# Performance work log

Hardware: AMD Instinct MI355X
Metric: run time of the kernel (lower is better)

Reference implementation:

```python
import jax, jax.numpy as jnp
import numpy as np

N = 8192          # number of bodies
BOX = 112.0       # world size chosen so expected #colliding pairs ~ 4N
EPS = 1e-12


def setup_inputs() -> dict:
    key = jax.random.key(0)
    k1, k2 = jax.random.split(key)
    centers = jax.random.uniform(k1, (N, 2), dtype=jnp.float32) * BOX
    radii = 0.5 + 0.5 * jax.random.uniform(k2, (N,), dtype=jnp.float32)
    return {"centers": centers, "radii": radii, "limit_broad": 4 * N, "limit_narrow": N}


def reference(centers, radii, limit_broad, limit_narrow):
    n = centers.shape[0]
    # ---- broad phase: all-pairs AABB overlap (AABB = center +/- radius) ----
    dc = jnp.abs(centers[:, None, :] - centers[None, :, :])      # [N,N,2]
    rsum = radii[:, None] + radii[None, :]                        # [N,N]
    overlap = jnp.all(dc <= rsum[..., None], axis=-1)             # [N,N]
    idx = jnp.arange(n)
    mask = overlap & (idx[:, None] < idx[None, :])                # i < j, as in _check_aabb_collision
    # compaction to a fixed limit of 4N candidate pairs (-1 = empty slot)
    flat = jnp.nonzero(mask.reshape(-1), size=limit_broad, fill_value=-1)[0]
    valid_b = flat >= 0
    safe = jnp.where(valid_b, flat, 0)
    pi, pj = safe // n, safe % n                                  # [4N]
    # ---- narrow phase: exact circle penetration on the candidates ----
    d = centers[pj] - centers[pi]                                 # [4N,2]
    dist = jnp.sqrt(jnp.sum(d * d, axis=-1) + EPS)                # [4N]
    depth = radii[pi] + radii[pj] - dist                          # [4N]
    pen = d / dist[:, None] * depth[:, None]                      # penetration vector [4N,2]
    hit = valid_b & (depth > 0)
    # second compaction: keep at most N actually-penetrating pairs
    sel = jnp.nonzero(hit, size=limit_narrow, fill_value=-1)[0]
    vsel = sel >= 0
    ssafe = jnp.where(vsel, sel, 0)
    si, sj = pi[ssafe], pj[ssafe]                                 # [N]
    delta = 0.5 * pen[ssafe] * vsel[:, None].astype(centers.dtype)
    # ---- resolve: scatter: push bodies apart by half the penetration each ----
    new_centers = centers.at[si].add(-delta).at[sj].add(delta)
    return new_centers
```

## Files before the change

### kernel.cpp

```cpp
#include <hip/hip_runtime.h>


constexpr int NB = 8192;
constexpr int GRID_DIM = 56;
constexpr int NCELLS = GRID_DIM * GRID_DIM;
constexpr int CAP = 20;
constexpr int BPB = 28;
constexpr int TPB9 = BPB * 9;
constexpr int NBLK9 = (NB + BPB - 1) / BPB;
constexpr float INV_CELL = 0.5f;
constexpr float EPS = 1e-12f;
constexpr int INF = 0x7fffffff;

constexpr int O_CCOUNT = 0;
constexpr int O_CSUM   = O_CCOUNT + NCELLS;
constexpr int O_BSUM   = O_CSUM + 32;
constexpr int O_SPEC   = O_BSUM + 32;
constexpr int O_POL    = O_SPEC + 8;
constexpr int O_COMB   = O_POL + NB / 4;
constexpr int O_CELLS  = (O_COMB + NB + 3) & ~3;
constexpr int MEMSET_INTS = O_SPEC + 8;

__device__ __forceinline__ int cell_of(float v) {
    int c = (int)(v * INV_CELL);
    return c > GRID_DIM - 1 ? GRID_DIM - 1 : (c < 0 ? 0 : c);
}

__device__ __forceinline__ int wave_incl_scan(int v, int lane) {
#pragma unroll
    for (int off = 1; off < 64; off <<= 1) {
        int y = __shfl_up(v, off);
        if (lane >= off) v += y;
    }
    return v;
}

__global__ void fill_kernel(const float2* __restrict__ centers,
                            const float* __restrict__ radii,
                            int* __restrict__ ccount,
                            float4* __restrict__ cells) {
    const int t = blockIdx.x * blockDim.x + threadIdx.x;
    if (t >= NB) return;
    const float2 c = centers[t];
    const int cell = cell_of(c.y) * GRID_DIM + cell_of(c.x);
    const int slot = atomicAdd(&ccount[cell], 1);
    if (slot < CAP)
        cells[cell * CAP + slot] = make_float4(c.x, c.y, radii[t], __int_as_float(t));
}

__global__ __launch_bounds__(256) void count_kernel(
        const float2* __restrict__ centers, const float* __restrict__ radii,
        const int* __restrict__ ccount, const float4* __restrict__ cells,
        int* __restrict__ comb, int* __restrict__ csum, int* __restrict__ bsum) {
    __shared__ int sh_c[256];
    __shared__ int sh_s[BPB];
    const int tid = threadIdx.x;
    const int local = tid / 9, cellk = tid - local * 9;
    const int b = blockIdx.x * BPB + local;
    int rc = 0, hc = 0;
    if (tid < TPB9 && b < NB) {
        const float2 ci = centers[b];
        const float ri = radii[b];
        const int cx = cell_of(ci.x), cy = cell_of(ci.y);
        const int xx = cx - 1 + cellk % 3, yy = cy - 1 + cellk / 3;
        if (xx >= 0 && xx < GRID_DIM && yy >= 0 && yy < GRID_DIM) {
            const int c = yy * GRID_DIM + xx;
            const int n = min(ccount[c], CAP);
            const float4* p = cells + c * CAP;
            for (int k = 0; k < n; ++k) {
                const float4 o = p[k];
                if (__float_as_int(o.w) <= b) continue;
                const float rs = ri + o.z;
                const float dx = o.x - ci.x, dy = o.y - ci.y;
                if (fabsf(dx) <= rs && fabsf(dy) <= rs) {
                    ++rc;
                    if (rs - sqrtf(dx * dx + dy * dy + EPS) > 0.f) ++hc;
                }
            }
        }
    }
    sh_c[tid] = (rc << 8) | hc;
    __syncthreads();
    if (cellk == 0 && tid < TPB9) {
        int s = 0;
#pragma unroll
        for (int k = 0; k < 9; ++k) s += sh_c[tid + k];
        if (b < NB) comb[b] = s;
        sh_s[local] = (b < NB) ? s : 0;
    }
    __syncthreads();
    if (tid == 0) {
        const int chunk0 = (blockIdx.x * BPB) >> 8;
        int sA = 0, sB = 0;
#pragma unroll
        for (int l = 0; l < BPB; ++l) {
            const int v = sh_s[l];
            const int w = (v >> 8 << 16) | (v & 0xff);
            if (((blockIdx.x * BPB + l) >> 8) == chunk0) sA += w; else sB += w;
        }
        atomicAdd(&bsum[chunk0], sA >> 16);
        atomicAdd(&csum[chunk0], sA & 0xffff);
        if (sB) {
            atomicAdd(&bsum[chunk0 + 1], sB >> 16);
            atomicAdd(&csum[chunk0 + 1], sB & 0xffff);
        }
    }
}

__device__ int2 pair_rank(const int* ccount, const float4* cells,
                          float xi, float yi, float ri, int i, int j, int blim) {
    const int cx = cell_of(xi), cy = cell_of(yi);
    const int x0 = max(cx - 1, 0), x1 = min(cx + 1, GRID_DIM - 1);
    const int y0 = max(cy - 1, 0), y1 = min(cy + 1, GRID_DIM - 1);
    int brank = 0, hrank = 0;
    for (int yy = y0; yy <= y1; ++yy)
        for (int xx = x0; xx <= x1; ++xx) {
            const int c = yy * GRID_DIM + xx;
            const int n = min(ccount[c], CAP);
            for (int k = 0; k < n; ++k) {
                const float4 o2 = cells[c * CAP + k];
                const int j2 = __float_as_int(o2.w);
                if (j2 <= i || j2 >= j) continue;
                const float rs2 = ri + o2.z;
                const float dx2 = o2.x - xi, dy2 = o2.y - yi;
                if (!(fabsf(dx2) <= rs2 && fabsf(dy2) <= rs2)) continue;
                ++brank;
                if (rs2 - sqrtf(dx2 * dx2 + dy2 * dy2 + EPS) > 0.f) {
                    if (blim == INF) ++hrank;
                    else {
                        int b2 = 0;
                        for (int yb = y0; yb <= y1; ++yb)
                            for (int xb = x0; xb <= x1; ++xb) {
                                const int cb2 = yb * GRID_DIM + xb;
                                const int nb2 = min(ccount[cb2], CAP);
                                for (int k2 = 0; k2 < nb2; ++k2) {
                                    const float4 o3 = cells[cb2 * CAP + k2];
                                    const int j3 = __float_as_int(o3.w);
                                    if (j3 <= i || j3 >= j2) continue;
                                    const float rs3 = ri + o3.z;
                                    if (fabsf(o3.x - xi) <= rs3 && fabsf(o3.y - yi) <= rs3)
                                        ++b2;
                                }
                            }
                        if (b2 < blim) ++hrank;
                    }
                }
            }
        }
    return make_int2(brank, hrank);
}

__device__ int slow_boundary_hits(const int* ccount, const float4* cells,
                                  const float2* centers, const float* radii,
                                  int i, int lim) {
    const float2 ci = centers[i];
    const float ri = radii[i];
    const int cx = cell_of(ci.x), cy = cell_of(ci.y);
    const int x0 = max(cx - 1, 0), x1 = min(cx + 1, GRID_DIM - 1);
    const int y0 = max(cy - 1, 0), y1 = min(cy + 1, GRID_DIM - 1);
    int h = 0;
    for (int yy = y0; yy <= y1; ++yy)
        for (int xx = x0; xx <= x1; ++xx) {
            const int c = yy * GRID_DIM + xx;
            const int n = min(ccount[c], CAP);
            for (int k = 0; k < n; ++k) {
                const float4 o = cells[c * CAP + k];
                const int j = __float_as_int(o.w);
                if (j <= i) continue;
                const float rs = ri + o.z, dx = o.x - ci.x, dy = o.y - ci.y;
                if (!(fabsf(dx) <= rs && fabsf(dy) <= rs)) continue;
                if (rs - sqrtf(dx * dx + dy * dy + EPS) <= 0.f) continue;
                const int2 r = pair_rank(ccount, cells, ci.x, ci.y, ri, i, j, INF);
                if (r.x < lim) ++h;
            }
        }
    return h;
}

__global__ __launch_bounds__(256) void pol_kernel(
        const float2* __restrict__ centers, const float* __restrict__ radii,
        const int* __restrict__ ccount, const float4* __restrict__ cells,
        const int* __restrict__ comb,
        const int* __restrict__ csum, const int* __restrict__ bsum,
        const int* __restrict__ LBp, const int* __restrict__ LNp,
        unsigned char* __restrict__ pol, int* __restrict__ spec) {
    __shared__ int sh_cs[32], sh_bs[32], wsum[4];
    const int tid = threadIdx.x, lane = tid & 63, wid = tid >> 6;
    const int blk = blockIdx.x;
    const int r = blk * 256 + tid;
    if (tid < 32) { sh_cs[tid] = csum[tid]; sh_bs[tid] = bsum[tid]; }
    __syncthreads();
    int hbase = 0, bbase = 0, btotal = 0;
#pragma unroll
    for (int c = 0; c < 32; ++c) {
        btotal += sh_bs[c];
        if (c < blk) { hbase += sh_cs[c]; bbase += sh_bs[c]; }
    }
    const int LB = *LBp, LN = *LNp;
    const int v = comb[r];
    const int rc = v >> 8, hr = v & 0xff;
    const int pk = (rc << 16) | hr;
    int incl = wave_incl_scan(pk, lane);
    if (lane == 63) wsum[wid] = incl;
    __syncthreads();
    if (wid == 0) {
        const int orig = (lane < 4) ? wsum[lane] : 0;
        const int inc = wave_incl_scan(orig, lane);
        if (lane < 4) wsum[lane] = inc - orig;
    }
    __syncthreads();
    const int excl = wsum[wid] + incl - pk;
    const int bstart = bbase + (excl >> 16);
    const int hstart = hbase + (excl & 0xffff);
    int hc = hr;
    if (btotal > LB) {
        if (bstart >= LB) hc = 0;
        else if (bstart + rc > LB)
            hc = slow_boundary_hits(ccount, cells, centers, radii, r, LB - bstart);
    }
    unsigned char p = 0;
    if (hc > 0 && hstart < LN) {
        const bool bf = (bstart + rc <= LB);
        const bool nf = (hstart + hc <= LN);
        if (bf && nf) p = 1;
        else {
            p = 2;
            if (!bf) {
                spec[2] = r + 1;
                spec[3] = LB - bstart;
                spec[4] = nf ? INF : LN - hstart;
            } else {
                spec[0] = r + 1;
                spec[1] = LN - hstart;
            }
        }
    }
    pol[r] = p;
}

__global__ __launch_bounds__(256) void gather_kernel(
        const float2* __restrict__ centers, const float* __restrict__ radii,
        const int* __restrict__ ccount, const float4* __restrict__ cells,
        const unsigned char* __restrict__ pol, const int* __restrict__ spec,
        float2* __restrict__ out) {
    __shared__ float sh_ax[256], sh_ay[256];
    __shared__ int sh_spec[5];
    const int tid = threadIdx.x;
    if (tid < 5) sh_spec[tid] = spec[tid];
    __syncthreads();
    const int sp0_row = sh_spec[0] - 1, sp0_hlim = sh_spec[1];
    const int sp1_row = sh_spec[2] - 1, sp1_blim = sh_spec[3], sp1_hlim = sh_spec[4];
    const int local = tid / 9, cellk = tid - local * 9;
    const int b = blockIdx.x * BPB + local;
    float ax = 0.f, ay = 0.f;
    if (tid < TPB9 && b < NB) {
        const float2 cb = centers[b];
        const float rb = radii[b];
        const unsigned char pol_b = pol[b];
        const int cx = cell_of(cb.x), cy = cell_of(cb.y);
        const int xx = cx - 1 + cellk % 3, yy = cy - 1 + cellk / 3;
        if (xx >= 0 && xx < GRID_DIM && yy >= 0 && yy < GRID_DIM) {
            const int c = yy * GRID_DIM + xx;
            const int n = min(ccount[c], CAP);
            const float4* p = cells + c * CAP;
            for (int k = 0; k < n; ++k) {
                const float4 o = p[k];
                const int id = __float_as_int(o.w);
                if (id == b) continue;
                const float rs = rb + o.z;
                const float dx = o.x - cb.x, dy = o.y - cb.y;
                if (!(fabsf(dx) <= rs && fabsf(dy) <= rs)) continue;
                const bool rowside = id > b;
                const unsigned char pq = rowside ? pol_b : pol[id];
                if (pq == 0) continue;
                const float dist = sqrtf(dx * dx + dy * dy + EPS);
                const float depth = rs - dist;
                if (depth <= 0.f) continue;
                bool apply = (pq == 1);
                if (!apply) {
                    const int ii = rowside ? b : id;
                    const int jj = rowside ? id : b;
                    int blim = INF, hlim = 0;
                    if (ii == sp1_row) { blim = sp1_blim; hlim = sp1_hlim; }
                    else if (ii == sp0_row) { hlim = sp0_hlim; }
                    const float xi = rowside ? cb.x : o.x;
                    const float yi = rowside ? cb.y : o.y;
                    const float ri = rowside ? rb : o.z;
                    const int2 rr = pair_rank(ccount, cells, xi, yi, ri, ii, jj, blim);
                    apply = (rr.x < blim) && (rr.y < hlim);
                }
                if (apply) {
                    const float sc = 0.5f * depth / dist;
                    ax -= sc * dx;
                    ay -= sc * dy;
                }
            }
        }
    }
    sh_ax[tid] = ax;
    sh_ay[tid] = ay;
    __syncthreads();
    if (cellk == 0 && tid < TPB9 && b < NB) {
        float sx = 0.f, sy = 0.f;
#pragma unroll
        for (int k = 0; k < 9; ++k) { sx += sh_ax[tid + k]; sy += sh_ay[tid + k]; }
        const float2 cb = centers[b];
        out[b] = make_float2(cb.x + sx, cb.y + sy);
    }
}

extern "C" void kernel_launch(void* const* d_in, const int* in_sizes, int n_in,
                              void* d_out, int out_size, void* d_ws, size_t ws_size,
                              hipStream_t stream) {
    const float2* centers = (const float2*)d_in[0];
    const float* radii    = (const float*)d_in[1];
    const int* LBp = (const int*)d_in[2];
    const int* LNp = (const int*)d_in[3];

    int* ws = (int*)d_ws;
    int* ccount = ws + O_CCOUNT;
    int* csum   = ws + O_CSUM;
    int* bsum   = ws + O_BSUM;
    int* spec   = ws + O_SPEC;
    unsigned char* pol = (unsigned char*)(ws + O_POL);
    int* comb   = ws + O_COMB;
    float4* cells = (float4*)(ws + O_CELLS);

    hipMemsetAsync(ws, 0, MEMSET_INTS * sizeof(int), stream);
    fill_kernel<<<NB / 256, 256, 0, stream>>>(centers, radii, ccount, cells);
    count_kernel<<<NBLK9, 256, 0, stream>>>(centers, radii, ccount, cells,
                                            comb, csum, bsum);
    pol_kernel<<<NB / 256, 256, 0, stream>>>(centers, radii, ccount, cells, comb,
                                             csum, bsum, LBp, LNp, pol, spec);
    gather_kernel<<<NBLK9, 256, 0, stream>>>(centers, radii, ccount, cells, pol,
                                             spec, (float2*)d_out);
}
```

Before: 103.5 us.

## Split cell scans across 18 threads and replace per-row policy with single-block scan

Count and gather kernels now use 18 threads per body, two per neighbour cell striding over slots, so each thread's serial loop is shorter and fewer bodies go in each block. The per-chunk atomic partial sums and the 32-block policy kernel are replaced by one single-block scan kernel. It scans all 8192 rows with 32 rows per thread and writes only the special boundary rows. Gather derives the apply rule from the boundary row indices instead of a per-row policy byte. This drops atomics and one buffer, at the cost of a serial single-block scan and more blocks in the gather and count passes.

```diff
diff --git a/kernel.cpp b/kernel.cpp
--- a/kernel.cpp
+++ b/kernel.cpp
@@ -5,21 +5,17 @@
 constexpr int GRID_DIM = 56;
 constexpr int NCELLS = GRID_DIM * GRID_DIM;
 constexpr int CAP = 20;
-constexpr int BPB = 28;
-constexpr int TPB9 = BPB * 9;
-constexpr int NBLK9 = (NB + BPB - 1) / BPB;
+constexpr int BPB = 14;
+constexpr int TPB18 = BPB * 18;
+constexpr int NBLK = (NB + BPB - 1) / BPB;
 constexpr float INV_CELL = 0.5f;
 constexpr float EPS = 1e-12f;
 constexpr int INF = 0x7fffffff;
 
 constexpr int O_CCOUNT = 0;
-constexpr int O_CSUM   = O_CCOUNT + NCELLS;
-constexpr int O_BSUM   = O_CSUM + 32;
-constexpr int O_SPEC   = O_BSUM + 32;
-constexpr int O_POL    = O_SPEC + 8;
-constexpr int O_COMB   = O_POL + NB / 4;
+constexpr int O_SPEC   = O_CCOUNT + NCELLS;
+constexpr int O_COMB   = O_SPEC + 8;
 constexpr int O_CELLS  = (O_COMB + NB + 3) & ~3;
-constexpr int MEMSET_INTS = O_SPEC + 8;
 
 __device__ __forceinline__ int cell_of(float v) {
     int c = (int)(v * INV_CELL);
@@ -51,23 +47,23 @@
 __global__ __launch_bounds__(256) void count_kernel(
         const float2* __restrict__ centers, const float* __restrict__ radii,
         const int* __restrict__ ccount, const float4* __restrict__ cells,
-        int* __restrict__ comb, int* __restrict__ csum, int* __restrict__ bsum) {
+        int* __restrict__ comb) {
     __shared__ int sh_c[256];
-    __shared__ int sh_s[BPB];
     const int tid = threadIdx.x;
-    const int local = tid / 9, cellk = tid - local * 9;
+    const int local = tid / 18, sub = tid - local * 18;
     const int b = blockIdx.x * BPB + local;
     int rc = 0, hc = 0;
-    if (tid < TPB9 && b < NB) {
+    if (tid < TPB18 && b < NB) {
         const float2 ci = centers[b];
         const float ri = radii[b];
         const int cx = cell_of(ci.x), cy = cell_of(ci.y);
+        const int cellk = sub >> 1, par = sub & 1;
         const int xx = cx - 1 + cellk % 3, yy = cy - 1 + cellk / 3;
         if (xx >= 0 && xx < GRID_DIM && yy >= 0 && yy < GRID_DIM) {
             const int c = yy * GRID_DIM + xx;
             const int n = min(ccount[c], CAP);
             const float4* p = cells + c * CAP;
-            for (int k = 0; k < n; ++k) {
+            for (int k = par; k < n; k += 2) {
                 const float4 o = p[k];
                 if (__float_as_int(o.w) <= b) continue;
                 const float rs = ri + o.z;
@@ -81,29 +77,11 @@
     }
     sh_c[tid] = (rc << 8) | hc;
     __syncthreads();
-    if (cellk == 0 && tid < TPB9) {
+    if (sub == 0 && tid < TPB18 && b < NB) {
         int s = 0;
 #pragma unroll
-        for (int k = 0; k < 9; ++k) s += sh_c[tid + k];
-        if (b < NB) comb[b] = s;
-        sh_s[local] = (b < NB) ? s : 0;
-    }
-    __syncthreads();
-    if (tid == 0) {
-        const int chunk0 = (blockIdx.x * BPB) >> 8;
-        int sA = 0, sB = 0;
-#pragma unroll
-        for (int l = 0; l < BPB; ++l) {
-            const int v = sh_s[l];
-            const int w = (v >> 8 << 16) | (v & 0xff);
-            if (((blockIdx.x * BPB + l) >> 8) == chunk0) sA += w; else sB += w;
-        }
-        atomicAdd(&bsum[chunk0], sA >> 16);
-        atomicAdd(&csum[chunk0], sA & 0xffff);
-        if (sB) {
-            atomicAdd(&bsum[chunk0 + 1], sB >> 16);
-            atomicAdd(&csum[chunk0 + 1], sB & 0xffff);
-        }
+        for (int k = 0; k < 18; ++k) s += sh_c[tid + k];
+        comb[b] = s;
     }
 }
 
@@ -177,30 +155,26 @@
     return h;
 }
 
-__global__ __launch_bounds__(256) void pol_kernel(
+__global__ __launch_bounds__(256) void scan_kernel(
         const float2* __restrict__ centers, const float* __restrict__ radii,
         const int* __restrict__ ccount, const float4* __restrict__ cells,
         const int* __restrict__ comb,
-        const int* __restrict__ csum, const int* __restrict__ bsum,
         const int* __restrict__ LBp, const int* __restrict__ LNp,
-        unsigned char* __restrict__ pol, int* __restrict__ spec) {
-    __shared__ int sh_cs[32], sh_bs[32], wsum[4];
+        int* __restrict__ spec) {
+    __shared__ int wsum[4];
+    __shared__ int sh_btot;
     const int tid = threadIdx.x, lane = tid & 63, wid = tid >> 6;
-    const int blk = blockIdx.x;
-    const int r = blk * 256 + tid;
-    if (tid < 32) { sh_cs[tid] = csum[tid]; sh_bs[tid] = bsum[tid]; }
-    __syncthreads();
-    int hbase = 0, bbase = 0, btotal = 0;
-#pragma unroll
-    for (int c = 0; c < 32; ++c) {
-        btotal += sh_bs[c];
-        if (c < blk) { hbase += sh_cs[c]; bbase += sh_bs[c]; }
-    }
-    const int LB = *LBp, LN = *LNp;
-    const int v = comb[r];
-    const int rc = v >> 8, hr = v & 0xff;
-    const int pk = (rc << 16) | hr;
-    int incl = wave_incl_scan(pk, lane);
+    if (tid == 0) { spec[0] = 0; spec[2] = 0; }
+    int crc[32];
+#pragma unroll
+    for (int k = 0; k < 8; ++k) {
+        const int4 v = ((const int4*)comb)[tid * 8 + k];
+        crc[4 * k] = v.x; crc[4 * k + 1] = v.y; crc[4 * k + 2] = v.z; crc[4 * k + 3] = v.w;
+    }
+    int rsum = 0;
+#pragma unroll
+    for (int k = 0; k < 32; ++k) rsum += crc[k] >> 8;
+    int incl = wave_incl_scan(rsum, lane);
     if (lane == 63) wsum[wid] = incl;
     __syncthreads();
     if (wid == 0) {
@@ -209,61 +183,88 @@
         if (lane < 4) wsum[lane] = inc - orig;
     }
     __syncthreads();
-    const int excl = wsum[wid] + incl - pk;
-    const int bstart = bbase + (excl >> 16);
-    const int hstart = hbase + (excl & 0xffff);
-    int hc = hr;
-    if (btotal > LB) {
-        if (bstart >= LB) hc = 0;
-        else if (bstart + rc > LB)
-            hc = slow_boundary_hits(ccount, cells, centers, radii, r, LB - bstart);
-    }
-    unsigned char p = 0;
-    if (hc > 0 && hstart < LN) {
-        const bool bf = (bstart + rc <= LB);
-        const bool nf = (hstart + hc <= LN);
-        if (bf && nf) p = 1;
-        else {
-            p = 2;
-            if (!bf) {
-                spec[2] = r + 1;
-                spec[3] = LB - bstart;
-                spec[4] = nf ? INF : LN - hstart;
-            } else {
-                spec[0] = r + 1;
-                spec[1] = LN - hstart;
-            }
-        }
-    }
-    pol[r] = p;
+    const int bstart0 = wsum[wid] + incl - rsum;
+    if (tid == 255) sh_btot = bstart0 + rsum;
+    __syncthreads();
+    const int btotal = sh_btot;
+    const int LB = *LBp, LN = *LNp;
+    int hcv[32];
+    int runb = bstart0, hsum = 0;
+#pragma unroll
+    for (int k = 0; k < 32; ++k) {
+        const int rc = crc[k] >> 8, hr = crc[k] & 0xff;
+        int hc = hr;
+        if (btotal > LB) {
+            if (runb >= LB) hc = 0;
+            else if (runb + rc > LB)
+                hc = slow_boundary_hits(ccount, cells, centers, radii,
+                                        tid * 32 + k, LB - runb);
+        }
+        hcv[k] = hc;
+        hsum += hc;
+        runb += rc;
+    }
+    __syncthreads();
+    incl = wave_incl_scan(hsum, lane);
+    if (lane == 63) wsum[wid] = incl;
+    __syncthreads();
+    if (wid == 0) {
+        const int orig = (lane < 4) ? wsum[lane] : 0;
+        const int inc = wave_incl_scan(orig, lane);
+        if (lane < 4) wsum[lane] = inc - orig;
+    }
+    __syncthreads();
+    int runh = wsum[wid] + incl - hsum;
+    runb = bstart0;
+#pragma unroll
+    for (int k = 0; k < 32; ++k) {
+        const int i = tid * 32 + k;
+        const int rc = crc[k] >> 8, hc = hcv[k];
+        if (hc > 0 && runh < LN) {
+            const bool bf = (runb + rc <= LB);
+            const bool nf = (runh + hc <= LN);
+            if (!(bf && nf)) {
+                if (!bf) {
+                    spec[2] = i + 1;
+                    spec[3] = LB - runb;
+                    spec[4] = nf ? INF : LN - runh;
+                } else {
+                    spec[0] = i + 1;
+                    spec[1] = LN - runh;
+                }
+            }
+        }
+        runb += rc;
+        runh += hc;
+    }
 }
 
 __global__ __launch_bounds__(256) void gather_kernel(
         const float2* __restrict__ centers, const float* __restrict__ radii,
         const int* __restrict__ ccount, const float4* __restrict__ cells,
-        const unsigned char* __restrict__ pol, const int* __restrict__ spec,
-        float2* __restrict__ out) {
+        const int* __restrict__ spec, float2* __restrict__ out) {
     __shared__ float sh_ax[256], sh_ay[256];
     __shared__ int sh_spec[5];
     const int tid = threadIdx.x;
     if (tid < 5) sh_spec[tid] = spec[tid];
     __syncthreads();
-    const int sp0_row = sh_spec[0] - 1, sp0_hlim = sh_spec[1];
-    const int sp1_row = sh_spec[2] - 1, sp1_blim = sh_spec[3], sp1_hlim = sh_spec[4];
-    const int local = tid / 9, cellk = tid - local * 9;
+    const int sp0 = sh_spec[0] - 1, sp0_hlim = sh_spec[1];
+    const int sp1 = sh_spec[2] - 1, sp1_blim = sh_spec[3], sp1_hlim = sh_spec[4];
+    const int lim1 = (sp0 >= 0) ? sp0 : ((sp1 >= 0) ? sp1 : NB);
+    const int local = tid / 18, sub = tid - local * 18;
     const int b = blockIdx.x * BPB + local;
     float ax = 0.f, ay = 0.f;
-    if (tid < TPB9 && b < NB) {
+    if (tid < TPB18 && b < NB) {
         const float2 cb = centers[b];
         const float rb = radii[b];
-        const unsigned char pol_b = pol[b];
         const int cx = cell_of(cb.x), cy = cell_of(cb.y);
+        const int cellk = sub >> 1, par = sub & 1;
         const int xx = cx - 1 + cellk % 3, yy = cy - 1 + cellk / 3;
         if (xx >= 0 && xx < GRID_DIM && yy >= 0 && yy < GRID_DIM) {
             const int c = yy * GRID_DIM + xx;
             const int n = min(ccount[c], CAP);
             const float4* p = cells + c * CAP;
-            for (int k = 0; k < n; ++k) {
+            for (int k = par; k < n; k += 2) {
                 const float4 o = p[k];
                 const int id = __float_as_int(o.w);
                 if (id == b) continue;
@@ -271,18 +272,17 @@
                 const float dx = o.x - cb.x, dy = o.y - cb.y;
                 if (!(fabsf(dx) <= rs && fabsf(dy) <= rs)) continue;
                 const bool rowside = id > b;
-                const unsigned char pq = rowside ? pol_b : pol[id];
-                if (pq == 0) continue;
+                const int ii = rowside ? b : id;
+                const bool special = (ii == sp0) | (ii == sp1);
+                if (ii >= lim1 && !special) continue;
                 const float dist = sqrtf(dx * dx + dy * dy + EPS);
                 const float depth = rs - dist;
                 if (depth <= 0.f) continue;
-                bool apply = (pq == 1);
-                if (!apply) {
-                    const int ii = rowside ? b : id;
+                bool apply = !special;
+                if (special) {
                     const int jj = rowside ? id : b;
-                    int blim = INF, hlim = 0;
-                    if (ii == sp1_row) { blim = sp1_blim; hlim = sp1_hlim; }
-                    else if (ii == sp0_row) { hlim = sp0_hlim; }
+                    const int blim = (ii == sp1) ? sp1_blim : INF;
+                    const int hlim = (ii == sp1) ? sp1_hlim : sp0_hlim;
                     const float xi = rowside ? cb.x : o.x;
                     const float yi = rowside ? cb.y : o.y;
                     const float ri = rowside ? rb : o.z;
@@ -300,10 +300,10 @@
     sh_ax[tid] = ax;
     sh_ay[tid] = ay;
     __syncthreads();
-    if (cellk == 0 && tid < TPB9 && b < NB) {
+    if (sub == 0 && tid < TPB18 && b < NB) {
         float sx = 0.f, sy = 0.f;
 #pragma unroll
-        for (int k = 0; k < 9; ++k) { sx += sh_ax[tid + k]; sy += sh_ay[tid + k]; }
+        for (int k = 0; k < 18; ++k) { sx += sh_ax[tid + k]; sy += sh_ay[tid + k]; }
         const float2 cb = centers[b];
         out[b] = make_float2(cb.x + sx, cb.y + sy);
     }
@@ -319,19 +319,15 @@
 
     int* ws = (int*)d_ws;
     int* ccount = ws + O_CCOUNT;
-    int* csum   = ws + O_CSUM;
-    int* bsum   = ws + O_BSUM;
     int* spec   = ws + O_SPEC;
-    unsigned char* pol = (unsigned char*)(ws + O_POL);
     int* comb   = ws + O_COMB;
     float4* cells = (float4*)(ws + O_CELLS);
 
-    hipMemsetAsync(ws, 0, MEMSET_INTS * sizeof(int), stream);
+    hipMemsetAsync(ccount, 0, NCELLS * sizeof(int), stream);
     fill_kernel<<<NB / 256, 256, 0, stream>>>(centers, radii, ccount, cells);
-    count_kernel<<<NBLK9, 256, 0, stream>>>(centers, radii, ccount, cells,
-                                            comb, csum, bsum);
-    pol_kernel<<<NB / 256, 256, 0, stream>>>(centers, radii, ccount, cells, comb,
-                                             csum, bsum, LBp, LNp, pol, spec);
-    gather_kernel<<<NBLK9, 256, 0, stream>>>(centers, radii, ccount, cells, pol,
-                                             spec, (float2*)d_out);
-}
+    count_kernel<<<NBLK, 256, 0, stream>>>(centers, radii, ccount, cells, comb);
+    scan_kernel<<<1, 256, 0, stream>>>(centers, radii, ccount, cells, comb,
+                                       LBp, LNp, spec);
+    gather_kernel<<<NBLK, 256, 0, stream>>>(centers, radii, ccount, cells,
+                                            spec, (float2*)d_out);
+}
```

Measured after the change: 91.91 us. 1.13x faster.
